# Optimization experiments

Measured on AMD Instinct MI355X. Metric: run time of the kernel, lower is better.

The kernel has to match this reference:

```python
import jax, jax.numpy as jnp
import numpy as np
from jax.scipy.linalg import expm

DIM = 1024


def setup_inputs() -> dict:
    key = jax.random.key(0)
    k1, k2 = jax.random.split(key)
    x = jax.random.normal(k1, (4, 4096, DIM), dtype=jnp.float32)
    skew_weights = jax.random.normal(k2, (DIM, DIM), dtype=jnp.float32) * 0.01
    return {"x": x, "skew_weights": skew_weights}


def reference(x, skew_weights):
    # A is skew-symmetric -> expm(A) is a rotation in SO(dim)
    A = skew_weights - skew_weights.T          # [dim, dim]
    R = expm(A)                                # [dim, dim]
    return jnp.matmul(x, R)                    # [..., dim] @ [dim, dim]
```

## Files before the change

kernel.cpp:

```cpp
#include <hip/hip_runtime.h>
#include <stdint.h>

#define DIM 1024
#define GLOBAL_AS __attribute__((address_space(1)))
#define LDS_AS __attribute__((address_space(3)))

typedef short bf16x8 __attribute__((ext_vector_type(8)));
typedef float f32x4 __attribute__((ext_vector_type(4)));

#define C3f 0.16666667f
#define C4f 0.041666668f

__device__ __forceinline__ unsigned short f32_to_bf16(float f) {
    union { float f; uint32_t u; } v; v.f = f;
    uint32_t u = v.u;
    u += 0x7FFFu + ((u >> 16) & 1u);
    return (unsigned short)(u >> 16);
}
__device__ __forceinline__ float bf16_to_f32(unsigned short u) {
    union { uint32_t u; float f; } v; v.u = ((uint32_t)u) << 16;
    return v.f;
}

__device__ __forceinline__ void async16(const void* g, void* l) {
    __builtin_amdgcn_global_load_lds((GLOBAL_AS const void*)g,
                                     (LDS_AS void*)l, 16, 0, 0);
}

__global__ __launch_bounds__(256) void k_initconv(const float* __restrict__ W,
        unsigned short* __restrict__ Ab, unsigned short* __restrict__ G,
        const float* __restrict__ X, unsigned short* __restrict__ Xb) {
    __shared__ float t2[32][33];
    int bid = blockIdx.x;
    int tid = threadIdx.x;
    if (bid >= 1024) {
        size_t id = (size_t)(bid - 1024) * 256 + tid;
        const f32x4* p = (const f32x4*)(X + id * 8);
        f32x4 v0 = p[0], v1 = p[1];
        unsigned short o[8];
        #pragma unroll
        for (int q = 0; q < 4; q++) { o[q] = f32_to_bf16(v0[q]); o[4 + q] = f32_to_bf16(v1[q]); }
        *(bf16x8*)&Xb[id * 8] = *(bf16x8*)o;
        return;
    }
    int i0 = (bid & 31) * 32, j0 = (bid >> 5) * 32;
    int tx = tid & 31, ty = tid >> 5;
    float t1[4];
    #pragma unroll
    for (int p = 0; p < 4; p++) {
        int r = p * 8 + ty;
        t1[p] = W[(i0 + r) * DIM + j0 + tx];
        t2[r][tx] = W[(j0 + r) * DIM + i0 + tx];
    }
    __syncthreads();
    #pragma unroll
    for (int p = 0; p < 4; p++) {
        int r = p * 8 + ty;
        float a = t1[p] - t2[tx][r];
        int gi = (i0 + r) * DIM + j0 + tx;
        Ab[gi] = f32_to_bf16(a);
        G[gi]  = f32_to_bf16(-a);
    }
}

template<int MODE>
__device__ __forceinline__ void gemm_chain_body(
        const unsigned short* __restrict__ P,
        const unsigned short* __restrict__ Qt,
        const unsigned short* __restrict__ Ab,
        const unsigned short* __restrict__ A2b,
        unsigned short* __restrict__ out1,
        unsigned short* __restrict__ out2) {
    int bid = blockIdx.x;
    int tid = threadIdx.x;
    __shared__ unsigned short lA[64 * 256];
    __shared__ unsigned short lB[64 * 256];
    int m0 = (bid & 15) * 64, n0 = (bid >> 4) * 64;
    int lane = tid & 63, w = tid >> 6;
    int wr = w >> 1, wc = w & 1;
    int rr = lane & 15, ko = lane >> 4;
    f32x4 acc[2][2] = {};
    for (int ks = 0; ks < 4; ks++) {
        int kb = ks * 256;
        #pragma unroll
        for (int i = 0; i < 8; i++) {
            int l = i * 256 + tid;
            int r = l >> 5, cst = l & 31;
            int cd = cst ^ (r & 7);
            async16(&P[(m0 + r) * DIM + kb + cd * 8], &lA[l * 8]);
            async16(&Qt[(n0 + r) * DIM + kb + cd * 8], &lB[l * 8]);
        }
        __syncthreads();
        #pragma unroll
        for (int s = 0; s < 8; s++) {
            int cd = s * 4 + ko;
            bf16x8 af[2], bq[2];
            #pragma unroll
            for (int mi = 0; mi < 2; mi++) {
                int ra = wr * 32 + mi * 16 + rr;
                af[mi] = *(const bf16x8*)&lA[ra * 256 + ((cd ^ (ra & 7)) * 8)];
            }
            #pragma unroll
            for (int ni = 0; ni < 2; ni++) {
                int rb = wc * 32 + ni * 16 + rr;
                bq[ni] = *(const bf16x8*)&lB[rb * 256 + ((cd ^ (rb & 7)) * 8)];
            }
            #pragma unroll
            for (int mi = 0; mi < 2; mi++)
                #pragma unroll
                for (int ni = 0; ni < 2; ni++)
                    acc[mi][ni] = __builtin_amdgcn_mfma_f32_16x16x32_bf16(
                        af[mi], bq[ni], acc[mi][ni], 0, 0, 0);
        }
        __syncthreads();
    }
    if (MODE == 1) {
        #pragma unroll
        for (int mi = 0; mi < 2; mi++)
            #pragma unroll
            for (int ni = 0; ni < 2; ni++)
                #pragma unroll
                for (int q = 0; q < 4; q++) {
                    int rl = wr * 32 + mi * 16 + ko * 4 + q;
                    int cl = wc * 32 + ni * 16 + rr;
                    int gi = (m0 + rl) * DIM + n0 + cl;
                    float v = acc[mi][ni][q];
                    out1[gi] = f32_to_bf16(v);
                    float a = bf16_to_f32(Ab[gi]);
                    out2[gi] = f32_to_bf16(C3f * a + C4f * v);
                }
    } else {
        float* tb = (float*)lA;
        #pragma unroll
        for (int mi = 0; mi < 2; mi++)
            #pragma unroll
            for (int ni = 0; ni < 2; ni++)
                #pragma unroll
                for (int q = 0; q < 4; q++) {
                    int rl = wr * 32 + mi * 16 + ko * 4 + q;
                    int cl = wc * 32 + ni * 16 + rr;
                    int gi = (m0 + rl) * DIM + n0 + cl;
                    float a = bf16_to_f32(Ab[gi]);
                    float a2 = bf16_to_f32(A2b[gi]);
                    float d = (m0 + rl == n0 + cl) ? 1.0f : 0.0f;
                    tb[cl * 65 + rl] = acc[mi][ni][q] + d + a + 0.5f * a2;
                }
        __syncthreads();
        #pragma unroll
        for (int q = 0; q < 16; q++) {
            int l = tid * 16 + q;
            int orow = l >> 6, ocol = l & 63;
            out1[(n0 + orow) * DIM + m0 + ocol] = f32_to_bf16(tb[orow * 65 + ocol]);
        }
    }
}

__global__ __launch_bounds__(256) void k_g1(
        const unsigned short* __restrict__ Ab, const unsigned short* __restrict__ G,
        unsigned short* __restrict__ A2b, unsigned short* __restrict__ Pb) {
    gemm_chain_body<1>(Ab, G, Ab, nullptr, A2b, Pb);
}

__global__ __launch_bounds__(256) void k_g2(
        const unsigned short* __restrict__ Pb, const unsigned short* __restrict__ A2b,
        const unsigned short* __restrict__ Ab, unsigned short* __restrict__ Rtb) {
    gemm_chain_body<2>(Pb, A2b, Ab, A2b, Rtb, nullptr);
}

__global__ __launch_bounds__(256, 4) void k_biggemm(
        const unsigned short* __restrict__ Xb,
        const unsigned short* __restrict__ Rtb,
        float* __restrict__ Out) {
    __shared__ unsigned short lX[128 * 64];
    __shared__ unsigned short lB[128 * 64];
    int tid = threadIdx.x;
    int bid = blockIdx.x;
    int m0 = (bid & 127) * 128, n0 = (bid >> 7) * 128;
    int lane = tid & 63, w = tid >> 6;
    int wr = w >> 1, wc = w & 1;
    int rr = lane & 15, ko = lane >> 4;
    f32x4 acc[4][4] = {};
    for (int kb = 0; kb < DIM; kb += 64) {
        #pragma unroll
        for (int i = 0; i < 4; i++) {
            int l = i * 256 + tid;
            int r = l >> 3, cst = l & 7;
            int cd = cst ^ (r & 7);
            async16(&Xb[(size_t)(m0 + r) * DIM + kb + cd * 8], &lX[l * 8]);
            async16(&Rtb[(n0 + r) * DIM + kb + cd * 8], &lB[l * 8]);
        }
        __syncthreads();
        #pragma unroll
        for (int s = 0; s < 2; s++) {
            int cd = s * 4 + ko;
            bf16x8 af[4], bq[4];
            #pragma unroll
            for (int mi = 0; mi < 4; mi++) {
                int ra = wr * 64 + mi * 16 + rr;
                af[mi] = *(const bf16x8*)&lX[ra * 64 + ((cd ^ (ra & 7)) * 8)];
            }
            #pragma unroll
            for (int ni = 0; ni < 4; ni++) {
                int rb = wc * 64 + ni * 16 + rr;
                bq[ni] = *(const bf16x8*)&lB[rb * 64 + ((cd ^ (rb & 7)) * 8)];
            }
            #pragma unroll
            for (int mi = 0; mi < 4; mi++)
                #pragma unroll
                for (int ni = 0; ni < 4; ni++)
                    acc[mi][ni] = __builtin_amdgcn_mfma_f32_16x16x32_bf16(
                        af[mi], bq[ni], acc[mi][ni], 0, 0, 0);
        }
        __syncthreads();
    }
    #pragma unroll
    for (int mi = 0; mi < 4; mi++)
        #pragma unroll
        for (int ni = 0; ni < 4; ni++)
            #pragma unroll
            for (int q = 0; q < 4; q++) {
                int row = m0 + wr * 64 + mi * 16 + ko * 4 + q;
                int col = n0 + wc * 64 + ni * 16 + rr;
                Out[(size_t)row * DIM + col] = acc[mi][ni][q];
            }
}

extern "C" void kernel_launch(void* const* d_in, const int* in_sizes, int n_in,
                              void* d_out, int out_size, void* d_ws, size_t ws_size,
                              hipStream_t stream) {
    const float* X = (const float*)d_in[0];
    const float* W = (const float*)d_in[1];
    float* Out = (float*)d_out;
    char* ws = (char*)d_ws;
    const size_t MB = 1u << 20;
    unsigned short* Ab  = (unsigned short*)(ws + 0 * MB);
    unsigned short* G   = (unsigned short*)(ws + 2 * MB);
    unsigned short* A2b = (unsigned short*)(ws + 4 * MB);
    unsigned short* Pb  = (unsigned short*)(ws + 6 * MB);
    unsigned short* Rtb = (unsigned short*)(ws + 8 * MB);
    unsigned short* Xb  = (unsigned short*)(ws + 10 * MB);

    k_initconv<<<1024 + 8192, 256, 0, stream>>>(W, Ab, G, X, Xb);
    k_g1<<<256, 256, 0, stream>>>(Ab, G, A2b, Pb);
    k_g2<<<256, 256, 0, stream>>>(Pb, A2b, Ab, Rtb);
    k_biggemm<<<1024, 256, 0, stream>>>(Xb, Rtb, Out);
}
```

Measured before the change: 164.8 us.

## Fuse init, both chain GEMMs and X conversion into one persistent kernel

Merges the skew/convert kernel and the two small 1024x1024 GEMM stages into one persistent kernel. Blocks 0-255 run the chain and synchronise through an atomic grid barrier, while blocks 256-511 convert X to bf16 in parallel. This is meant to remove two kernel launch gaps and let the X conversion overlap the small GEMMs. It relies on all 512 blocks being co-resident for the spin barrier (deadlock risk otherwise) and adds a memset launch.

Result: slower. 242.0 us (+46.9%).

```diff
diff --git a/kernel.cpp b/kernel.cpp
--- a/kernel.cpp
+++ b/kernel.cpp
@@ -27,94 +27,115 @@
                                      (LDS_AS void*)l, 16, 0, 0);
 }
 
-__global__ __launch_bounds__(256) void k_initconv(const float* __restrict__ W,
+__device__ __forceinline__ void gbar(unsigned* ctr, unsigned target) {
+    __syncthreads();
+    if (threadIdx.x == 0) {
+        __threadfence();
+        __hip_atomic_fetch_add(ctr, 1u, __ATOMIC_ACQ_REL,
+                               __HIP_MEMORY_SCOPE_AGENT);
+        while (__hip_atomic_load(ctr, __ATOMIC_ACQUIRE,
+                                 __HIP_MEMORY_SCOPE_AGENT) < target)
+            __builtin_amdgcn_s_sleep(8);
+        __threadfence();
+    }
+    __syncthreads();
+}
+
+__global__ __launch_bounds__(256, 2) void k_chain(
+        const float* __restrict__ W, const float* __restrict__ X,
         unsigned short* __restrict__ Ab, unsigned short* __restrict__ G,
-        const float* __restrict__ X, unsigned short* __restrict__ Xb) {
-    __shared__ float t2[32][33];
-    int bid = blockIdx.x;
-    int tid = threadIdx.x;
-    if (bid >= 1024) {
-        size_t id = (size_t)(bid - 1024) * 256 + tid;
-        const f32x4* p = (const f32x4*)(X + id * 8);
-        f32x4 v0 = p[0], v1 = p[1];
-        unsigned short o[8];
-        #pragma unroll
-        for (int q = 0; q < 4; q++) { o[q] = f32_to_bf16(v0[q]); o[4 + q] = f32_to_bf16(v1[q]); }
-        *(bf16x8*)&Xb[id * 8] = *(bf16x8*)o;
+        unsigned short* __restrict__ A2b, unsigned short* __restrict__ Pb,
+        unsigned short* __restrict__ Rtb, unsigned short* __restrict__ Xb,
+        unsigned* __restrict__ bar) {
+    int bid = blockIdx.x, tid = threadIdx.x;
+
+    if (bid >= 256) {
+        int b = bid - 256;
+        #pragma unroll 4
+        for (int it = 0; it < 32; it++) {
+            size_t id = (size_t)it * 65536 + (size_t)b * 256 + tid;
+            const f32x4* p = (const f32x4*)(X + id * 8);
+            f32x4 v0 = p[0], v1 = p[1];
+            unsigned short o[8];
+            #pragma unroll
+            for (int q = 0; q < 4; q++) { o[q] = f32_to_bf16(v0[q]); o[4 + q] = f32_to_bf16(v1[q]); }
+            *(bf16x8*)&Xb[id * 8] = *(bf16x8*)o;
+        }
         return;
     }
-    int i0 = (bid & 31) * 32, j0 = (bid >> 5) * 32;
-    int tx = tid & 31, ty = tid >> 5;
-    float t1[4];
-    #pragma unroll
-    for (int p = 0; p < 4; p++) {
-        int r = p * 8 + ty;
-        t1[p] = W[(i0 + r) * DIM + j0 + tx];
-        t2[r][tx] = W[(j0 + r) * DIM + i0 + tx];
-    }
-    __syncthreads();
-    #pragma unroll
-    for (int p = 0; p < 4; p++) {
-        int r = p * 8 + ty;
-        float a = t1[p] - t2[tx][r];
-        int gi = (i0 + r) * DIM + j0 + tx;
-        Ab[gi] = f32_to_bf16(a);
-        G[gi]  = f32_to_bf16(-a);
-    }
-}
-
-template<int MODE>
-__device__ __forceinline__ void gemm_chain_body(
-        const unsigned short* __restrict__ P,
-        const unsigned short* __restrict__ Qt,
-        const unsigned short* __restrict__ Ab,
-        const unsigned short* __restrict__ A2b,
-        unsigned short* __restrict__ out1,
-        unsigned short* __restrict__ out2) {
-    int bid = blockIdx.x;
-    int tid = threadIdx.x;
+
     __shared__ unsigned short lA[64 * 256];
     __shared__ unsigned short lB[64 * 256];
-    int m0 = (bid & 15) * 64, n0 = (bid >> 4) * 64;
     int lane = tid & 63, w = tid >> 6;
     int wr = w >> 1, wc = w & 1;
     int rr = lane & 15, ko = lane >> 4;
-    f32x4 acc[2][2] = {};
-    for (int ks = 0; ks < 4; ks++) {
-        int kb = ks * 256;
-        #pragma unroll
-        for (int i = 0; i < 8; i++) {
-            int l = i * 256 + tid;
-            int r = l >> 5, cst = l & 31;
-            int cd = cst ^ (r & 7);
-            async16(&P[(m0 + r) * DIM + kb + cd * 8], &lA[l * 8]);
-            async16(&Qt[(n0 + r) * DIM + kb + cd * 8], &lB[l * 8]);
-        }
-        __syncthreads();
-        #pragma unroll
-        for (int s = 0; s < 8; s++) {
-            int cd = s * 4 + ko;
-            bf16x8 af[2], bq[2];
-            #pragma unroll
-            for (int mi = 0; mi < 2; mi++) {
-                int ra = wr * 32 + mi * 16 + rr;
-                af[mi] = *(const bf16x8*)&lA[ra * 256 + ((cd ^ (ra & 7)) * 8)];
-            }
-            #pragma unroll
-            for (int ni = 0; ni < 2; ni++) {
-                int rb = wc * 32 + ni * 16 + rr;
-                bq[ni] = *(const bf16x8*)&lB[rb * 256 + ((cd ^ (rb & 7)) * 8)];
-            }
-            #pragma unroll
-            for (int mi = 0; mi < 2; mi++)
-                #pragma unroll
-                for (int ni = 0; ni < 2; ni++)
-                    acc[mi][ni] = __builtin_amdgcn_mfma_f32_16x16x32_bf16(
-                        af[mi], bq[ni], acc[mi][ni], 0, 0, 0);
-        }
-        __syncthreads();
-    }
-    if (MODE == 1) {
+
+    {
+        float (*t2)[33] = (float(*)[33])lA;
+        int tx = tid & 31, ty = tid >> 5;
+        #pragma unroll
+        for (int rep = 0; rep < 4; rep++) {
+            int tile = bid * 4 + rep;
+            int i0 = (tile & 31) * 32, j0 = (tile >> 5) * 32;
+            float t1[4];
+            #pragma unroll
+            for (int p = 0; p < 4; p++) {
+                int r = p * 8 + ty;
+                t1[p] = W[(i0 + r) * DIM + j0 + tx];
+                t2[r][tx] = W[(j0 + r) * DIM + i0 + tx];
+            }
+            __syncthreads();
+            #pragma unroll
+            for (int p = 0; p < 4; p++) {
+                int r = p * 8 + ty;
+                float a = t1[p] - t2[tx][r];
+                int gi = (i0 + r) * DIM + j0 + tx;
+                Ab[gi] = f32_to_bf16(a);
+                G[gi]  = f32_to_bf16(-a);
+            }
+            __syncthreads();
+        }
+    }
+    gbar(bar, 256);
+
+    int m0 = (bid & 15) * 64, n0 = (bid >> 4) * 64;
+
+    {
+        f32x4 acc[2][2] = {};
+        for (int ks = 0; ks < 4; ks++) {
+            int kb = ks * 256;
+            #pragma unroll
+            for (int i = 0; i < 8; i++) {
+                int l = i * 256 + tid;
+                int r = l >> 5, cst = l & 31;
+                int cd = cst ^ (r & 7);
+                async16(&Ab[(m0 + r) * DIM + kb + cd * 8], &lA[l * 8]);
+                async16(&G[(n0 + r) * DIM + kb + cd * 8], &lB[l * 8]);
+            }
+            __syncthreads();
+            #pragma unroll
+            for (int s = 0; s < 8; s++) {
+                int cd = s * 4 + ko;
+                bf16x8 af[2], bq[2];
+                #pragma unroll
+                for (int mi = 0; mi < 2; mi++) {
+                    int ra = wr * 32 + mi * 16 + rr;
+                    af[mi] = *(const bf16x8*)&lA[ra * 256 + ((cd ^ (ra & 7)) * 8)];
+                }
+                #pragma unroll
+                for (int ni = 0; ni < 2; ni++) {
+                    int rb = wc * 32 + ni * 16 + rr;
+                    bq[ni] = *(const bf16x8*)&lB[rb * 256 + ((cd ^ (rb & 7)) * 8)];
+                }
+                #pragma unroll
+                for (int mi = 0; mi < 2; mi++)
+                    #pragma unroll
+                    for (int ni = 0; ni < 2; ni++)
+                        acc[mi][ni] = __builtin_amdgcn_mfma_f32_16x16x32_bf16(
+                            af[mi], bq[ni], acc[mi][ni], 0, 0, 0);
+            }
+            __syncthreads();
+        }
         #pragma unroll
         for (int mi = 0; mi < 2; mi++)
             #pragma unroll
@@ -125,11 +146,49 @@
                     int cl = wc * 32 + ni * 16 + rr;
                     int gi = (m0 + rl) * DIM + n0 + cl;
                     float v = acc[mi][ni][q];
-                    out1[gi] = f32_to_bf16(v);
+                    A2b[gi] = f32_to_bf16(v);
                     float a = bf16_to_f32(Ab[gi]);
-                    out2[gi] = f32_to_bf16(C3f * a + C4f * v);
-                }
-    } else {
+                    Pb[gi] = f32_to_bf16(C3f * a + C4f * v);
+                }
+    }
+    gbar(bar, 512);
+
+    {
+        f32x4 acc[2][2] = {};
+        for (int ks = 0; ks < 4; ks++) {
+            int kb = ks * 256;
+            #pragma unroll
+            for (int i = 0; i < 8; i++) {
+                int l = i * 256 + tid;
+                int r = l >> 5, cst = l & 31;
+                int cd = cst ^ (r & 7);
+                async16(&Pb[(m0 + r) * DIM + kb + cd * 8], &lA[l * 8]);
+                async16(&A2b[(n0 + r) * DIM + kb + cd * 8], &lB[l * 8]);
+            }
+            __syncthreads();
+            #pragma unroll
+            for (int s = 0; s < 8; s++) {
+                int cd = s * 4 + ko;
+                bf16x8 af[2], bq[2];
+                #pragma unroll
+                for (int mi = 0; mi < 2; mi++) {
+                    int ra = wr * 32 + mi * 16 + rr;
+                    af[mi] = *(const bf16x8*)&lA[ra * 256 + ((cd ^ (ra & 7)) * 8)];
+                }
+                #pragma unroll
+                for (int ni = 0; ni < 2; ni++) {
+                    int rb = wc * 32 + ni * 16 + rr;
+                    bq[ni] = *(const bf16x8*)&lB[rb * 256 + ((cd ^ (rb & 7)) * 8)];
+                }
+                #pragma unroll
+                for (int mi = 0; mi < 2; mi++)
+                    #pragma unroll
+                    for (int ni = 0; ni < 2; ni++)
+                        acc[mi][ni] = __builtin_amdgcn_mfma_f32_16x16x32_bf16(
+                            af[mi], bq[ni], acc[mi][ni], 0, 0, 0);
+            }
+            __syncthreads();
+        }
         float* tb = (float*)lA;
         #pragma unroll
         for (int mi = 0; mi < 2; mi++)
@@ -150,21 +209,9 @@
         for (int q = 0; q < 16; q++) {
             int l = tid * 16 + q;
             int orow = l >> 6, ocol = l & 63;
-            out1[(n0 + orow) * DIM + m0 + ocol] = f32_to_bf16(tb[orow * 65 + ocol]);
-        }
-    }
-}
-
-__global__ __launch_bounds__(256) void k_g1(
-        const unsigned short* __restrict__ Ab, const unsigned short* __restrict__ G,
-        unsigned short* __restrict__ A2b, unsigned short* __restrict__ Pb) {
-    gemm_chain_body<1>(Ab, G, Ab, nullptr, A2b, Pb);
-}
-
-__global__ __launch_bounds__(256) void k_g2(
-        const unsigned short* __restrict__ Pb, const unsigned short* __restrict__ A2b,
-        const unsigned short* __restrict__ Ab, unsigned short* __restrict__ Rtb) {
-    gemm_chain_body<2>(Pb, A2b, Ab, A2b, Rtb, nullptr);
+            Rtb[(n0 + orow) * DIM + m0 + ocol] = f32_to_bf16(tb[orow * 65 + ocol]);
+        }
+    }
 }
 
 __global__ __launch_bounds__(256, 4) void k_biggemm(
@@ -239,9 +286,9 @@
     unsigned short* Pb  = (unsigned short*)(ws + 6 * MB);
     unsigned short* Rtb = (unsigned short*)(ws + 8 * MB);
     unsigned short* Xb  = (unsigned short*)(ws + 10 * MB);
-
-    k_initconv<<<1024 + 8192, 256, 0, stream>>>(W, Ab, G, X, Xb);
-    k_g1<<<256, 256, 0, stream>>>(Ab, G, A2b, Pb);
-    k_g2<<<256, 256, 0, stream>>>(Pb, A2b, Ab, Rtb);
+    unsigned* bar = (unsigned*)(ws + 42 * MB);
+
+    hipMemsetAsync(bar, 0, 8, stream);
+    k_chain<<<512, 256, 0, stream>>>(W, X, Ab, G, A2b, Pb, Rtb, Xb, bar);
     k_biggemm<<<1024, 256, 0, stream>>>(Xb, Rtb, Out);
 }
```
